# Optimization experiments

Measured on AMD Instinct MI355X. Metric: run time of the kernel, lower is better.

The kernel has to match this reference:

```python
import jax, jax.numpy as jnp
import numpy as np

WIN_SIZE = 9  # (2*win_rad+1)^2 with win_rad=1
EPS = 1e-7   # compute_laplacian default eps


def _windows(a):
    """Sliding 3x3 window extraction: (H, W, ...) -> (H-2, W-2, 9, ...)."""
    H, W = a.shape[0], a.shape[1]
    ch, cw = H - 2, W - 2
    return jnp.stack([a[dy:dy + ch, dx:dx + cw] for dy in range(3) for dx in range(3)], axis=2)


def _laplacian_vals(img):
    """Per-window matting Laplacian blocks. img: (H, W, 3) -> vals: (N, 9, 9)."""
    winI = _windows(img).reshape(-1, WIN_SIZE, 3)                      # (N, 9, 3)
    mu = winI.mean(axis=1, keepdims=True)                              # (N, 1, 3)
    var = (jnp.einsum('nji,njk->nik', winI, winI) / WIN_SIZE
           - jnp.einsum('nji,njk->nik', mu, mu))                       # (N, 3, 3)
    inv = jnp.linalg.inv(var + (EPS / WIN_SIZE) * jnp.eye(3, dtype=img.dtype))
    Xc = winI - mu                                                     # (N, 9, 3)
    X = jnp.einsum('nij,njk->nik', Xc, inv)                            # (N, 9, 3)
    vals = jnp.eye(WIN_SIZE, dtype=img.dtype) - (1.0 + jnp.einsum('nij,nkj->nik', X, Xc)) / WIN_SIZE
    return vals                                                        # (N, 9, 9)


def _win_inds(H, W):
    """Flat pixel indices of each 3x3 window: (N, 9) int32. Static given H, W."""
    idx = jnp.arange(H * W, dtype=jnp.int32).reshape(H, W)
    return _windows(idx).reshape(-1, WIN_SIZE)


def setup_inputs() -> dict:
    key = jax.random.key(0)
    k1, k2 = jax.random.split(key)
    B, C, H, W = 4, 3, 512, 512
    output = jax.random.normal(k1, (B, C, H, W), dtype=jnp.float32)
    content = jax.random.uniform(k2, (B, C, H, W), dtype=jnp.float32)
    return {"output": output, "content": content}


def reference(output, content):
    B, C, H, W = output.shape
    img = jnp.moveaxis(content, 1, 3)          # (B, H, W, 3)
    inds = _win_inds(H, W)                     # (N, 9) constant index map

    def per_image(im, out):
        vals = _laplacian_vals(im)             # (N, 9, 9)
        xw = out.reshape(C, H * W)[:, inds]    # (C, N, 9) gather per window
        # sum over channels/windows of x_win^T L_win x_win == sum_c x_c^T L x_c
        return jnp.einsum('nij,cni,cnj->', vals, xw, xw)

    loss = jax.vmap(per_image)(img, output)    # (B,)
    return loss.reshape(B, 1, 1)
```

## Files before the change

kernel.cpp:

```cpp
#include <hip/hip_runtime.h>

#define EPSV 1e-7f

typedef float f2 __attribute__((ext_vector_type(2)));

__global__ __launch_bounds__(256) void matting_loss_kernel(
    const float* __restrict__ outp, const float* __restrict__ cont,
    float* __restrict__ ws)
{
    const int H = 512, W = 512, NW = 510;
    const int HW = H * W;

    const int lin = blockIdx.x + 8 * (blockIdx.y + 32 * blockIdx.z);
    const int swz = (lin & 7) * 128 + (lin >> 3);
    const int b   = swz >> 8;
    const int rem = swz & 255;
    const int gx  = (rem & 7) * 32 + threadIdx.x;
    const int gg  = (rem >> 3) * 8 + threadIdx.y;
    const int wx0 = gx * 2;
    const int wy0 = gg * 2;

    const float* Cin = cont + (size_t)b * 3 * HW;
    const float* Xin = outp + (size_t)b * 3 * HW;

    float contrib = 0.0f;
    const float inv9 = 1.0f / 9.0f;

#define WSUM(OUT, A0, A1) { f2 T_ = (A0) + (A1); (OUT).x = T_.x + (A0).y; (OUT).y = T_.y + (A1).x; }
#define CSUM(CH, R0, OUT) { \
    f2 A0_ = Cb[CH][R0][0] + Cb[CH][R0+1][0] + Cb[CH][R0+2][0]; \
    f2 A1_ = Cb[CH][R0][1] + Cb[CH][R0+1][1] + Cb[CH][R0+2][1]; \
    WSUM(OUT, A0_, A1_) }
#define CDOT(CA, CB_, R0, OUT) { \
    f2 A0_ = Cb[CA][R0][0]*Cb[CB_][R0][0] + Cb[CA][R0+1][0]*Cb[CB_][R0+1][0] + Cb[CA][R0+2][0]*Cb[CB_][R0+2][0]; \
    f2 A1_ = Cb[CA][R0][1]*Cb[CB_][R0][1] + Cb[CA][R0+1][1]*Cb[CB_][R0+1][1] + Cb[CA][R0+2][1]*Cb[CB_][R0+2][1]; \
    WSUM(OUT, A0_, A1_) }
#define XSUM(R0, OUT) { \
    f2 A0_ = Xb[R0][0] + Xb[R0+1][0] + Xb[R0+2][0]; \
    f2 A1_ = Xb[R0][1] + Xb[R0+1][1] + Xb[R0+2][1]; \
    WSUM(OUT, A0_, A1_) }
#define XXDOT(R0, OUT) { \
    f2 A0_ = Xb[R0][0]*Xb[R0][0] + Xb[R0+1][0]*Xb[R0+1][0] + Xb[R0+2][0]*Xb[R0+2][0]; \
    f2 A1_ = Xb[R0][1]*Xb[R0][1] + Xb[R0+1][1]*Xb[R0+1][1] + Xb[R0+2][1]*Xb[R0+2][1]; \
    WSUM(OUT, A0_, A1_) }
#define XCDOT(R0, K_, OUT) { \
    f2 A0_ = Xb[R0][0]*Cb[K_][R0][0] + Xb[R0+1][0]*Cb[K_][R0+1][0] + Xb[R0+2][0]*Cb[K_][R0+2][0]; \
    f2 A1_ = Xb[R0][1]*Cb[K_][R0][1] + Xb[R0+1][1]*Cb[K_][R0+1][1] + Xb[R0+2][1]*Cb[K_][R0+2][1]; \
    WSUM(OUT, A0_, A1_) }

    if (wy0 < NW && wx0 < NW) {
        const int base = wy0 * W + wx0;

        f2 Cb[3][4][2];
        #pragma unroll
        for (int ch = 0; ch < 3; ++ch)
            #pragma unroll
            for (int r = 0; r < 4; ++r) {
                const float* p = Cin + ch * HW + base + r * W;
                Cb[ch][r][0] = *(const f2*)p;
                Cb[ch][r][1] = *(const f2*)(p + 2);
            }

        f2 mu0[2], mu1[2], mu2[2];
        f2 adj0[2], adj1[2], adj2[2], adj3[2], adj4[2], adj5[2], idet[2];
        #pragma unroll
        for (int wr = 0; wr < 2; ++wr) {
            f2 sI0, sI1, sI2, s00, s01, s02, s11, s12, s22;
            CSUM(0, wr, sI0) CSUM(1, wr, sI1) CSUM(2, wr, sI2)
            CDOT(0, 0, wr, s00) CDOT(0, 1, wr, s01) CDOT(0, 2, wr, s02)
            CDOT(1, 1, wr, s11) CDOT(1, 2, wr, s12) CDOT(2, 2, wr, s22)
            f2 m0 = sI0 * inv9, m1 = sI1 * inv9, m2 = sI2 * inv9;
            const float ed = EPSV * inv9;
            f2 v00 = s00 * inv9 - m0 * m0 + ed;
            f2 v01 = s01 * inv9 - m0 * m1;
            f2 v02 = s02 * inv9 - m0 * m2;
            f2 v11 = s11 * inv9 - m1 * m1 + ed;
            f2 v12 = s12 * inv9 - m1 * m2;
            f2 v22 = s22 * inv9 - m2 * m2 + ed;
            f2 a0 = v11 * v22 - v12 * v12;
            f2 a1 = v02 * v12 - v01 * v22;
            f2 a2 = v01 * v12 - v02 * v11;
            f2 det = v00 * a0 + v01 * a1 + v02 * a2;
            mu0[wr] = m0; mu1[wr] = m1; mu2[wr] = m2;
            adj0[wr] = a0; adj1[wr] = a1; adj2[wr] = a2;
            adj3[wr] = v00 * v22 - v02 * v02;
            adj4[wr] = v01 * v02 - v00 * v12;
            adj5[wr] = v00 * v11 - v01 * v01;
            f2 idv;
            idv.x = __builtin_amdgcn_rcpf(det.x);
            idv.y = __builtin_amdgcn_rcpf(det.y);
            idet[wr] = idv;
        }

        f2 termAcc = (f2){0.0f, 0.0f};
        #pragma unroll
        for (int c = 0; c < 3; ++c) {
            f2 Xb[4][2];
            #pragma unroll
            for (int r = 0; r < 4; ++r) {
                const float* q = Xin + c * HW + base + r * W;
                Xb[r][0] = *(const f2*)q;
                Xb[r][1] = *(const f2*)(q + 2);
            }
            #pragma unroll
            for (int wr = 0; wr < 2; ++wr) {
                f2 S, SSw, W0, W1, W2;
                XSUM(wr, S) XXDOT(wr, SSw)
                XCDOT(wr, 0, W0) XCDOT(wr, 1, W1) XCDOT(wr, 2, W2)
                f2 u0 = W0 - S * mu0[wr];
                f2 u1 = W1 - S * mu1[wr];
                f2 u2 = W2 - S * mu2[wr];
                f2 qa = u0 * (adj0[wr] * u0 + adj1[wr] * u1 + adj2[wr] * u2)
                      + u1 * (adj1[wr] * u0 + adj3[wr] * u1 + adj4[wr] * u2)
                      + u2 * (adj2[wr] * u0 + adj4[wr] * u1 + adj5[wr] * u2);
                termAcc += SSw - (S * S + qa * idet[wr]) * inv9;
            }
        }
        contrib = termAcc.x + termAcc.y;
    }
#undef WSUM
#undef CSUM
#undef CDOT
#undef XSUM
#undef XXDOT
#undef XCDOT

    #pragma unroll
    for (int off = 32; off > 0; off >>= 1)
        contrib += __shfl_down(contrib, off, 64);

    __shared__ float wsum[4];
    const int tid = threadIdx.y * 32 + threadIdx.x;
    const int lane = tid & 63, wv = tid >> 6;
    if (lane == 0) wsum[wv] = contrib;
    __syncthreads();
    if (tid == 0)
        ws[swz] = wsum[0] + wsum[1] + wsum[2] + wsum[3];
}

__global__ __launch_bounds__(256) void reduce_kernel(
    const float* __restrict__ ws, float* __restrict__ loss)
{
    const int b = blockIdx.x;
    const int t = threadIdx.x;
    float v = ws[b * 256 + t];
    #pragma unroll
    for (int off = 32; off > 0; off >>= 1)
        v += __shfl_down(v, off, 64);

    __shared__ float s[4];
    if ((t & 63) == 0) s[t >> 6] = v;
    __syncthreads();
    if (t == 0) loss[b] = s[0] + s[1] + s[2] + s[3];
}

extern "C" void kernel_launch(void* const* d_in, const int* in_sizes, int n_in,
                              void* d_out, int out_size, void* d_ws, size_t ws_size,
                              hipStream_t stream) {
    const float* outp = (const float*)d_in[0];
    const float* cont = (const float*)d_in[1];
    float* loss = (float*)d_out;
    float* ws   = (float*)d_ws;

    dim3 block(32, 8, 1);
    dim3 grid(8, 32, 4);
    matting_loss_kernel<<<grid, block, 0, stream>>>(outp, cont, ws);
    reduce_kernel<<<dim3(4, 1, 1), dim3(256, 1, 1), 0, stream>>>(ws, loss);
}
```

Baseline: 13.78 us.

## Stage content and output tiles in shared memory with halo

```diff
diff --git a/kernel.cpp b/kernel.cpp
--- a/kernel.cpp
+++ b/kernel.cpp
@@ -4,24 +4,54 @@
 
 typedef float f2 __attribute__((ext_vector_type(2)));
 
-__global__ __launch_bounds__(256) void matting_loss_kernel(
+__global__ __launch_bounds__(512) void matting_loss_kernel(
     const float* __restrict__ outp, const float* __restrict__ cont,
     float* __restrict__ ws)
 {
-    const int H = 512, W = 512, NW = 510;
-    const int HW = H * W;
+    const int HW = 512 * 512;
 
-    const int lin = blockIdx.x + 8 * (blockIdx.y + 32 * blockIdx.z);
-    const int swz = (lin & 7) * 128 + (lin >> 3);
-    const int b   = swz >> 8;
-    const int rem = swz & 255;
-    const int gx  = (rem & 7) * 32 + threadIdx.x;
-    const int gg  = (rem >> 3) * 8 + threadIdx.y;
-    const int wx0 = gx * 2;
-    const int wy0 = gg * 2;
+    const int lin = blockIdx.x + 8 * (blockIdx.y + 16 * blockIdx.z);
+    const int swz = (lin & 7) * 64 + (lin >> 3);
+    const int b   = swz >> 7;
+    const int rem = swz & 127;
+    const int by  = rem >> 3;
+    const int bx  = rem & 7;
+
+    const int tx = threadIdx.x;
+    const int ty = threadIdx.y;
+    const int rowBase = by * 32;
+    const int colBase = bx * 64;
 
     const float* Cin = cont + (size_t)b * 3 * HW;
     const float* Xin = outp + (size_t)b * 3 * HW;
+
+    __shared__ float sC[3][34][68];
+    __shared__ float sX[3][34][68];
+
+    #pragma unroll
+    for (int ch = 0; ch < 3; ++ch) {
+        #pragma unroll
+        for (int rr = 0; rr < 3; ++rr) {
+            const int r = ty + 16 * rr;
+            if (rr < 2 || ty < 2) {
+                const int grow = rowBase + r;
+                if (grow < 512) {
+                    const float* pc = Cin + ch * HW + grow * 512 + colBase;
+                    const float* px = Xin + ch * HW + grow * 512 + colBase;
+                    *(f2*)&sC[ch][r][2 * tx] = *(const f2*)(pc + 2 * tx);
+                    *(f2*)&sX[ch][r][2 * tx] = *(const f2*)(px + 2 * tx);
+                    if (tx == 0 && colBase + 65 < 512) {
+                        *(f2*)&sC[ch][r][64] = *(const f2*)(pc + 64);
+                        *(f2*)&sX[ch][r][64] = *(const f2*)(px + 64);
+                    }
+                }
+            }
+        }
+    }
+    __syncthreads();
+
+    const int wy0 = rowBase + 2 * ty;
+    const int wx0 = colBase + 2 * tx;
 
     float contrib = 0.0f;
     const float inv9 = 1.0f / 9.0f;
@@ -48,17 +78,14 @@
     f2 A1_ = Xb[R0][1]*Cb[K_][R0][1] + Xb[R0+1][1]*Cb[K_][R0+1][1] + Xb[R0+2][1]*Cb[K_][R0+2][1]; \
     WSUM(OUT, A0_, A1_) }
 
-    if (wy0 < NW && wx0 < NW) {
-        const int base = wy0 * W + wx0;
-
+    if (wy0 < 510 && wx0 < 510) {
         f2 Cb[3][4][2];
         #pragma unroll
         for (int ch = 0; ch < 3; ++ch)
             #pragma unroll
             for (int r = 0; r < 4; ++r) {
-                const float* p = Cin + ch * HW + base + r * W;
-                Cb[ch][r][0] = *(const f2*)p;
-                Cb[ch][r][1] = *(const f2*)(p + 2);
+                Cb[ch][r][0] = *(const f2*)&sC[ch][2 * ty + r][2 * tx];
+                Cb[ch][r][1] = *(const f2*)&sC[ch][2 * ty + r][2 * tx + 2];
             }
 
         f2 mu0[2], mu1[2], mu2[2];
@@ -98,9 +125,8 @@
             f2 Xb[4][2];
             #pragma unroll
             for (int r = 0; r < 4; ++r) {
-                const float* q = Xin + c * HW + base + r * W;
-                Xb[r][0] = *(const f2*)q;
-                Xb[r][1] = *(const f2*)(q + 2);
+                Xb[r][0] = *(const f2*)&sX[c][2 * ty + r][2 * tx];
+                Xb[r][1] = *(const f2*)&sX[c][2 * ty + r][2 * tx + 2];
             }
             #pragma unroll
             for (int wr = 0; wr < 2; ++wr) {
@@ -129,29 +155,33 @@
     for (int off = 32; off > 0; off >>= 1)
         contrib += __shfl_down(contrib, off, 64);
 
-    __shared__ float wsum[4];
-    const int tid = threadIdx.y * 32 + threadIdx.x;
+    __shared__ float wsum[8];
+    const int tid = ty * 32 + tx;
     const int lane = tid & 63, wv = tid >> 6;
     if (lane == 0) wsum[wv] = contrib;
     __syncthreads();
-    if (tid == 0)
-        ws[swz] = wsum[0] + wsum[1] + wsum[2] + wsum[3];
+    if (tid == 0) {
+        float s = 0.0f;
+        #pragma unroll
+        for (int w = 0; w < 8; ++w) s += wsum[w];
+        ws[swz] = s;
+    }
 }
 
-__global__ __launch_bounds__(256) void reduce_kernel(
+__global__ __launch_bounds__(128) void reduce_kernel(
     const float* __restrict__ ws, float* __restrict__ loss)
 {
     const int b = blockIdx.x;
     const int t = threadIdx.x;
-    float v = ws[b * 256 + t];
+    float v = ws[b * 128 + t];
     #pragma unroll
     for (int off = 32; off > 0; off >>= 1)
         v += __shfl_down(v, off, 64);
 
-    __shared__ float s[4];
+    __shared__ float s[2];
     if ((t & 63) == 0) s[t >> 6] = v;
     __syncthreads();
-    if (t == 0) loss[b] = s[0] + s[1] + s[2] + s[3];
+    if (t == 0) loss[b] = s[0] + s[1];
 }
 
 extern "C" void kernel_launch(void* const* d_in, const int* in_sizes, int n_in,
@@ -162,8 +192,8 @@
     float* loss = (float*)d_out;
     float* ws   = (float*)d_ws;
 
-    dim3 block(32, 8, 1);
-    dim3 grid(8, 32, 4);
+    dim3 block(32, 16, 1);
+    dim3 grid(8, 16, 4);
     matting_loss_kernel<<<grid, block, 0, stream>>>(outp, cont, ws);
-    reduce_kernel<<<dim3(4, 1, 1), dim3(256, 1, 1), 0, stream>>>(ws, loss);
+    reduce_kernel<<<dim3(4, 1, 1), dim3(128, 1, 1), 0, stream>>>(ws, loss);
 }
```

Measured after the change: 16.83 us. +22.1%, slower.
